# Kernel optimization log

Hardware: AMD Instinct MI355X
Metric: run time of the kernel (lower is better)

Reference implementation:

```python
import jax, jax.numpy as jnp
import numpy as np

N_FILTRATIONS = 24
TEMPERATURE = 0.15
H1_WEIGHT = 0.5
LAMBDA_TOPO = 0.1


def setup_inputs() -> dict:
    key = jax.random.key(0)
    embeddings = jax.random.normal(key, (4096, 512), dtype=jnp.float32)
    return {"embeddings": embeddings, "step": 0}


def _landscape_loss(embeddings):
    N = embeddings.shape[0]
    emb = embeddings.astype(jnp.float32)
    # pairwise euclidean distances (torch.cdist p=2), safe sqrt for grad at 0
    sq = jnp.sum(emb * emb, axis=1)
    d2 = sq[:, None] + sq[None, :] - 2.0 * (emb @ emb.T)
    d2 = jnp.maximum(d2, 0.0)
    pos = d2 > 1e-12
    dist = jnp.where(pos, jnp.sqrt(jnp.where(pos, d2, 1.0)), 0.0)
    eye = jnp.eye(N, dtype=jnp.float32)
    dist = dist + eye * 1e9  # [N, N], diag pushed to 'infinity'
    off = dist < 1e8
    # thresholds come from .item() in torch -> no grad through them
    d_min = jax.lax.stop_gradient(jnp.min(jnp.where(off, dist, jnp.inf)))
    d_max = jax.lax.stop_gradient(
        jnp.maximum(jnp.max(jnp.where(off, dist, -jnp.inf)), d_min + 1e-4))
    thresholds = jnp.linspace(d_min, d_max, N_FILTRATIONS)

    one_minus_eye = 1.0 - eye

    def step_fn(carry, thresh):
        adj = jax.nn.sigmoid((thresh - dist) / TEMPERATURE) * one_minus_eye
        deg = jnp.clip(jnp.sum(adj, axis=-1), 1e-6, None)
        n_isolated = jnp.sum((deg < 0.5).astype(jnp.float32))  # H0 proxy
        n_edges_soft = jnp.sum(adj) / 2.0
        n_excess = jax.nn.relu(n_edges_soft - (N - 1)) / N  # H1 proxy
        return carry, (n_isolated, n_excess)

    _, (h0, h1) = jax.lax.scan(step_fn, None, thresholds)
    h0_loss = jnp.mean(h0[-8:])
    h1_loss = jnp.mean(h1)
    total = h0_loss + H1_WEIGHT * h1_loss
    return total * LAMBDA_TOPO


def reference(embeddings, step) -> jnp.ndarray:
    # warmup_steps = 0, so the warmup skip branch never triggers;
    # N == max_points, so no subsampling.
    return _landscape_loss(embeddings)
```

## Files before the change

kernel.cpp:

```cpp
#include <hip/hip_runtime.h>
#include <stdint.h>

typedef float f32x4 __attribute__((ext_vector_type(4)));
typedef short s16x8 __attribute__((ext_vector_type(8)));
typedef unsigned short us4 __attribute__((ext_vector_type(4)));

#define NPTS 4096
#define DDIM 512
#define NF   24
#define NBLK 32
#define NBD  1024

#define OFF_SQ  4194304
#define OFF_MM  4210688
#define OFF_DEG 4210752
#define OFF_D   4603968
#define OFF_H   38158400ULL
#define WS_A    54935616ULL

typedef __attribute__((address_space(1))) void gvoid;
typedef __attribute__((address_space(3))) void svoid;
#define GLD16(gp, lp) __builtin_amdgcn_global_load_lds((gvoid*)(gp), (svoid*)(lp), 16, 0, 0)

static __device__ __forceinline__ ushort f2h(float x) {
    _Float16 h = (_Float16)x;
    return __builtin_bit_cast(unsigned short, h);
}
static __device__ __forceinline__ float h2f(ushort u) {
    return (float)__builtin_bit_cast(_Float16, u);
}

__global__ __launch_bounds__(256) void k_init(float* __restrict__ deg,
                                              unsigned* __restrict__ mm) {
    int i = blockIdx.x * 256 + threadIdx.x;
    if (i < NPTS * NF) deg[i] = 0.0f;
    if (i == 0) { mm[0] = 0x7F7FFFFFu; mm[1] = 0u; }
}

__global__ __launch_bounds__(256) void k_convert(const float* __restrict__ in,
                                                 ushort* __restrict__ Eb,
                                                 float* __restrict__ sq,
                                                 float* __restrict__ acc32,
                                                 unsigned* __restrict__ mm) {
    if (blockIdx.x == 0) {
        if (threadIdx.x < 32) acc32[threadIdx.x] = 0.0f;
        else if (threadIdx.x == 32) mm[0] = 0x7F7FFFFFu;
        else if (threadIdx.x == 33) mm[1] = 0u;
    }
    const int w = threadIdx.x >> 6, lane = threadIdx.x & 63;
    const int row = blockIdx.x * 4 + w;
    const float* src = in + (size_t)row * DDIM + lane * 8;
    float4 a = ((const float4*)src)[0];
    float4 b = ((const float4*)src)[1];
    float v[8] = {a.x, a.y, a.z, a.w, b.x, b.y, b.z, b.w};
    unsigned u[8];
    float ss = 0.0f;
#pragma unroll
    for (int i = 0; i < 8; ++i) {
        ss += v[i] * v[i];
        unsigned bits = __float_as_uint(v[i]);
        u[i] = (bits + 0x7FFFu + ((bits >> 16) & 1u)) >> 16;
    }
    uint4 pk;
    pk.x = u[0] | (u[1] << 16);
    pk.y = u[2] | (u[3] << 16);
    pk.z = u[4] | (u[5] << 16);
    pk.w = u[6] | (u[7] << 16);
    *(uint4*)(Eb + (size_t)row * DDIM + lane * 8) = pk;
#pragma unroll
    for (int s = 1; s < 64; s <<= 1) ss += __shfl_xor(ss, s);
    if (lane == 0) sq[row] = ss;
}

__global__ __launch_bounds__(256) void k_gram_bk64(const ushort* __restrict__ Eb,
                                                   const float* __restrict__ sq,
                                                   unsigned* __restrict__ mm,
                                                   ushort* __restrict__ D2h) {
    __shared__ __align__(16) ushort SM[32768];
    __shared__ float sqr[128], sqc[128], red[8];
    char* SMb = (char*)SM;
    const int tid = threadIdx.x;
    const int w = tid >> 6, lane = tid & 63, g = lane >> 4, l15 = lane & 15;
    const int wr = w >> 1, wc = w & 1;

    int bid = (blockIdx.x & 7) * 66 + (blockIdx.x >> 3);
    int rb = 0, pre = 0;
    while (pre + (NBLK - rb) <= bid) { pre += NBLK - rb; ++rb; }
    const int cb = rb + (bid - pre);

    if (tid < 128) sqr[tid] = sq[rb * 128 + tid];
    else           sqc[tid - 128] = sq[cb * 128 + (tid - 128)];

    f32x4 acc[4][4];
#pragma unroll
    for (int i = 0; i < 4; ++i)
#pragma unroll
        for (int j = 0; j < 4; ++j) acc[i][j] = (f32x4){0.f, 0.f, 0.f, 0.f};

    const int srow_off = lane >> 3, slch = lane & 7;

#define STAGE64(buf, kk)                                                        \
    {                                                                           \
        const int k0_ = (kk) * 64;                                              \
        _Pragma("unroll")                                                       \
        for (int i_ = 0; i_ < 4; ++i_) {                                        \
            const int r_  = w * 32 + i_ * 8 + srow_off;                         \
            const int ch_ = slch ^ (r_ & 7);                                    \
            GLD16(Eb + (size_t)(rb * 128 + r_) * DDIM + k0_ + ch_ * 8,          \
                  SMb + (buf) * 16384 + (w * 32 + i_ * 8) * 128);               \
            GLD16(Eb + (size_t)(cb * 128 + r_) * DDIM + k0_ + ch_ * 8,          \
                  SMb + 32768 + (buf) * 16384 + (w * 32 + i_ * 8) * 128);       \
        }                                                                       \
    }

    STAGE64(0, 0);
    int cur = 0;
#pragma unroll 1
    for (int kk = 0; kk < 8; ++kk) {
        __syncthreads();
        if (kk < 7) STAGE64(cur ^ 1, kk + 1);
        const char* Ac = SMb + cur * 16384;
        const char* Bc = SMb + 32768 + cur * 16384;
#pragma unroll
        for (int ks = 0; ks < 2; ++ks) {
            s16x8 rf[4], cf[4];
#pragma unroll
            for (int i = 0; i < 4; ++i) {
                const int r = wr * 64 + i * 16 + l15;
                const int slot = (ks * 4 + g) ^ (r & 7);
                rf[i] = *(const s16x8*)(Ac + r * 128 + slot * 16);
            }
#pragma unroll
            for (int j = 0; j < 4; ++j) {
                const int r = wc * 64 + j * 16 + l15;
                const int slot = (ks * 4 + g) ^ (r & 7);
                cf[j] = *(const s16x8*)(Bc + r * 128 + slot * 16);
            }
#pragma unroll
            for (int i = 0; i < 4; ++i)
#pragma unroll
                for (int j = 0; j < 4; ++j)
                    acc[i][j] = __builtin_amdgcn_mfma_f32_16x16x32_bf16(
                        cf[j], rf[i], acc[i][j], 0, 0, 0);
        }
        cur ^= 1;
    }
    __syncthreads();

    ushort* T = SM;
    float mn = 3.4e38f, mx = 0.0f;
#pragma unroll
    for (int i = 0; i < 4; ++i) {
        const int lr = wr * 64 + i * 16 + l15;
        const int trow = rb * 128 + lr;
        const float srv = sqr[lr];
#pragma unroll
        for (int j = 0; j < 4; ++j) {
            const int c0 = wc * 64 + j * 16 + g * 4;
            const int tc0 = cb * 128 + c0;
            ushort h[4];
#pragma unroll
            for (int m = 0; m < 4; ++m) {
                float d2 = srv + sqc[c0 + m] - 2.0f * acc[i][j][m];
                d2 = fmaxf(d2, 0.0f);
                bool diag = (tc0 + m == trow);
                mn = diag ? mn : fminf(mn, d2);
                mx = diag ? mx : fmaxf(mx, d2);
                h[m] = f2h(diag ? 6.0e4f : d2);
            }
            us4 pk4 = {h[0], h[1], h[2], h[3]};
            *(us4*)(T + lr * 136 + c0) = pk4;
        }
    }
#pragma unroll
    for (int s = 1; s < 64; s <<= 1) {
        mn = fminf(mn, __shfl_xor(mn, s));
        mx = fmaxf(mx, __shfl_xor(mx, s));
    }
    if (lane == 0) { red[w] = mn; red[4 + w] = mx; }
    __syncthreads();
    if (tid == 0) {
        mn = fminf(fminf(red[0], red[1]), fminf(red[2], red[3]));
        mx = fmaxf(fmaxf(red[4], red[5]), fmaxf(red[6], red[7]));
        atomicMin(&mm[0], __float_as_uint(mn));
        atomicMax(&mm[1], __float_as_uint(mx));
    }
#pragma unroll
    for (int j = 0; j < 8; ++j) {
        const int c = j * 256 + tid;
        const int row = c >> 4, col8 = (c & 15) * 8;
        uint4 v = *(const uint4*)(T + row * 136 + col8);
        *(uint4*)(D2h + (size_t)(rb * 128 + row) * NPTS + cb * 128 + col8) = v;
    }
    if (rb != cb) {
        __syncthreads();
#pragma unroll
        for (int i = 0; i < 4; ++i) {
            const int lr = wr * 64 + i * 16 + l15;
            const float srv = sqr[lr];
#pragma unroll
            for (int j = 0; j < 4; ++j) {
                const int c0 = wc * 64 + j * 16 + g * 4;
#pragma unroll
                for (int m = 0; m < 4; ++m) {
                    float d2 = srv + sqc[c0 + m] - 2.0f * acc[i][j][m];
                    d2 = fmaxf(d2, 0.0f);
                    T[(c0 + m) * 136 + lr] = f2h(d2);
                }
            }
        }
        __syncthreads();
#pragma unroll
        for (int j2 = 0; j2 < 8; ++j2) {
            const int c = j2 * 256 + tid;
            const int row = c >> 4, col8 = (c & 15) * 8;
            uint4 v = *(const uint4*)(T + row * 136 + col8);
            *(uint4*)(D2h + (size_t)(cb * 128 + row) * NPTS + rb * 128 + col8) = v;
        }
    }
}

__global__ __launch_bounds__(256) void k_hist4(const ushort* __restrict__ D2h,
                                               const unsigned* __restrict__ mm,
                                               ushort* __restrict__ H) {
    __shared__ unsigned Hs[4][NBD + 4];
    const int tid = threadIdx.x, w = tid >> 6, lane = tid & 63;
    const int row0 = blockIdx.x * 4;
    const int row = row0 + w;
    for (int i = tid; i < 4 * (NBD + 4); i += 256) ((unsigned*)Hs)[i] = 0u;
    const float d2min = __uint_as_float(mm[0]);
    const float d2max = __uint_as_float(mm[1]);
    const float sc = (float)NBD / fmaxf(d2max - d2min, 1e-6f);
    __syncthreads();
    const uint4* Dv = (const uint4*)(D2h + (size_t)row * NPTS);
    unsigned* hr = Hs[w];
#pragma unroll
    for (int it = 0; it < 8; ++it) {
        uint4 pk = Dv[it * 64 + lane];
        unsigned pw[4] = {pk.x, pk.y, pk.z, pk.w};
#pragma unroll
        for (int i = 0; i < 4; ++i) {
            float a = h2f((ushort)(pw[i] & 0xFFFFu));
            float b = h2f((ushort)(pw[i] >> 16));
            if (a < 3.0e4f) {
                int ba = (int)fminf(fmaxf((a - d2min) * sc, 0.0f), (float)(NBD - 1));
                atomicAdd(&hr[ba], 1u);
            }
            if (b < 3.0e4f) {
                int bb = (int)fminf(fmaxf((b - d2min) * sc, 0.0f), (float)(NBD - 1));
                atomicAdd(&hr[bb], 1u);
            }
        }
    }
    __syncthreads();
    unsigned* Ho = (unsigned*)(H + (size_t)row0 * NBD);
    for (int i = tid; i < 4 * (NBD / 2); i += 256) {
        const int r = i >> 9, pw_ = i & 511;
        unsigned lo = Hs[r][2 * pw_], hi = Hs[r][2 * pw_ + 1];
        Ho[r * (NBD / 2) + pw_] = (lo & 0xFFFFu) | (hi << 16);
    }
}

__global__ __launch_bounds__(512) void k_dot(const ushort* __restrict__ H,
                                             const unsigned* __restrict__ mm,
                                             float* __restrict__ acc32) {
    __shared__ float Wl[4][NBD];
    __shared__ float degb[8][NF];
    const int tid = threadIdx.x;
    const int wid = tid >> 6, lane = tid & 63;
    const int row = blockIdx.x * 8 + wid;

    const float d2min = __uint_as_float(mm[0]);
    const float d2max = __uint_as_float(mm[1]);
    const float bw    = fmaxf(d2max - d2min, 1e-6f) / (float)NBD;
    const float d_min = d2min > 1e-12f ? sqrtf(d2min) : 0.0f;
    const float d_mx  = d2max > 1e-12f ? sqrtf(d2max) : 0.0f;
    const float d_max = fmaxf(d_mx, d_min + 1e-4f);
    const float stp   = (d_max - d_min) / 23.0f;
    const float S2L   = (1.0f / 0.15f) * 1.44269504f;
    const float Ds2   = stp * S2L;
    const float R     = exp2f(-Ds2);
    const float LIM   = 1073741824.0f;

    float hv[16];
    const ushort* Hr = H + (size_t)row * NBD;
#pragma unroll
    for (int j = 0; j < 4; ++j) {
        uint2 pk = *(const uint2*)(Hr + j * 256 + lane * 4);
        hv[j * 4 + 0] = (float)(pk.x & 0xFFFFu);
        hv[j * 4 + 1] = (float)(pk.x >> 16);
        hv[j * 4 + 2] = (float)(pk.y & 0xFFFFu);
        hv[j * 4 + 3] = (float)(pk.y >> 16);
    }

    float e2[2];
#pragma unroll
    for (int q = 0; q < 2; ++q) {
        const int b = tid * 2 + q;
        const float d2c = d2min + ((float)b + 0.5f) * bw;
        const float db = sqrtf(fmaxf(d2c, 0.0f));
        e2[q] = exp2f(fminf((db - d_min) * S2L, 125.0f));
    }

#pragma unroll 1
    for (int ph = 0; ph < 6; ++ph) {
        __syncthreads();
#pragma unroll
        for (int k = 0; k < 4; ++k) {
            float2 sg;
            sg.x = __builtin_amdgcn_rcpf(1.0f + fminf(e2[0], LIM)); e2[0] *= R;
            sg.y = __builtin_amdgcn_rcpf(1.0f + fminf(e2[1], LIM)); e2[1] *= R;
            *(float2*)(&Wl[k][tid * 2]) = sg;
        }
        __syncthreads();
        float dacc[4];
#pragma unroll
        for (int k = 0; k < 4; ++k) {
            const float* Wr = &Wl[k][0];
            float s = 0.0f;
#pragma unroll
            for (int j = 0; j < 4; ++j) {
                const f32x4 wv = *(const f32x4*)(Wr + j * 256 + lane * 4);
                s += hv[j*4+0]*wv[0] + hv[j*4+1]*wv[1] + hv[j*4+2]*wv[2] + hv[j*4+3]*wv[3];
            }
            dacc[k] = s;
        }
#pragma unroll
        for (int k = 0; k < 4; ++k)
#pragma unroll
            for (int o = 1; o < 64; o <<= 1) dacc[k] += __shfl_xor(dacc[k], o);
        if (lane == 0) {
#pragma unroll
            for (int k = 0; k < 4; ++k) degb[wid][ph * 4 + k] = dacc[k];
        }
    }
    __syncthreads();
    if (tid < NF) {
        float s = 0.0f;
#pragma unroll
        for (int r = 0; r < 8; ++r) s += degb[r][tid];
        atomicAdd(&acc32[tid], s);
    } else if (tid < 32) {
        const int k = 16 + (tid - NF);
        float c = 0.0f;
#pragma unroll
        for (int r = 0; r < 8; ++r) c += (degb[r][k] < 0.5f) ? 1.0f : 0.0f;
        atomicAdd(&acc32[tid], c);
    }
}

__global__ __launch_bounds__(64) void k_final2(const float* __restrict__ acc32,
                                               float* __restrict__ out) {
    if (threadIdx.x == 0) {
        float h1 = 0.0f;
#pragma unroll
        for (int k = 0; k < NF; ++k)
            h1 += fmaxf(acc32[k] * 0.5f - (float)(NPTS - 1), 0.0f) * (1.0f / (float)NPTS);
        float h0 = 0.0f;
#pragma unroll
        for (int k = 0; k < 8; ++k) h0 += acc32[NF + k];
        out[0] = (h0 * 0.125f + 0.5f * (h1 * (1.0f / 24.0f))) * 0.1f;
    }
}

__device__ __forceinline__ void gram_tile(const ushort* __restrict__ Eb, int rb, int cb,
                                          ushort* As, ushort* Bs, f32x4 acc[2][8]) {
    const int tid = threadIdx.x;
    const int w = tid >> 6, lane = tid & 63, g = lane >> 4, l15 = lane & 15;
#pragma unroll 1
    for (int kk = 0; kk < DDIM / 32; ++kk) {
        const int k0 = kk * 32;
        __syncthreads();
#pragma unroll
        for (int it = 0; it < 2; ++it) {
            int li  = it * 256 + tid;
            int row = li >> 2, ch = li & 3;
            uint4 va = *(const uint4*)(Eb + (size_t)(rb * 128 + row) * DDIM + k0 + ch * 8);
            uint4 vb = *(const uint4*)(Eb + (size_t)(cb * 128 + row) * DDIM + k0 + ch * 8);
            *(uint4*)(As + row * 32 + ch * 8) = va;
            *(uint4*)(Bs + row * 32 + ch * 8) = vb;
        }
        __syncthreads();
        s16x8 rf0 = *(const s16x8*)(As + (w * 32 + 0 * 16 + l15) * 32 + g * 8);
        s16x8 rf1 = *(const s16x8*)(As + (w * 32 + 1 * 16 + l15) * 32 + g * 8);
#pragma unroll
        for (int bj = 0; bj < 8; ++bj) {
            s16x8 cf = *(const s16x8*)(Bs + (bj * 16 + l15) * 32 + g * 8);
            acc[0][bj] = __builtin_amdgcn_mfma_f32_16x16x32_bf16(cf, rf0, acc[0][bj], 0, 0, 0);
            acc[1][bj] = __builtin_amdgcn_mfma_f32_16x16x32_bf16(cf, rf1, acc[1][bj], 0, 0, 0);
        }
    }
}

__global__ __launch_bounds__(256) void k_minmax(const ushort* __restrict__ Eb,
                                                const float* __restrict__ sq,
                                                unsigned* __restrict__ mm) {
    const int rb = blockIdx.y, cb = blockIdx.x;
    if (cb < rb) return;
    __shared__ ushort As[128 * 32], Bs[128 * 32];
    __shared__ float sqr[128], sqc[128];
    __shared__ float red[8];
    const int tid = threadIdx.x;
    if (tid < 128) sqr[tid] = sq[rb * 128 + tid];
    else           sqc[tid - 128] = sq[cb * 128 + (tid - 128)];
    f32x4 acc[2][8];
#pragma unroll
    for (int bi = 0; bi < 2; ++bi)
#pragma unroll
        for (int bj = 0; bj < 8; ++bj) acc[bi][bj] = (f32x4){0.f, 0.f, 0.f, 0.f};
    gram_tile(Eb, rb, cb, As, Bs, acc);
    const int w = tid >> 6, lane = tid & 63, g = lane >> 4, l15 = lane & 15;
    const float sr0 = sqr[w * 32 + l15], sr1 = sqr[w * 32 + 16 + l15];
    float mn = 3.4e38f, mx = 0.0f;
#pragma unroll
    for (int bi = 0; bi < 2; ++bi)
#pragma unroll
        for (int bj = 0; bj < 8; ++bj)
#pragma unroll
            for (int m = 0; m < 4; ++m) {
                int tr = w * 32 + bi * 16 + l15;
                int tc = bj * 16 + g * 4 + m;
                float d2 = (bi ? sr1 : sr0) + sqc[tc] - 2.0f * acc[bi][bj][m];
                d2 = fmaxf(d2, 0.0f);
                bool diag = (rb == cb) && (tr == tc);
                mn = diag ? mn : fminf(mn, d2);
                mx = diag ? mx : fmaxf(mx, d2);
            }
#pragma unroll
    for (int s = 1; s < 64; s <<= 1) {
        mn = fminf(mn, __shfl_xor(mn, s));
        mx = fmaxf(mx, __shfl_xor(mx, s));
    }
    if (lane == 0) { red[w] = mn; red[4 + w] = mx; }
    __syncthreads();
    if (tid == 0) {
        mn = fminf(fminf(red[0], red[1]), fminf(red[2], red[3]));
        mx = fmaxf(fmaxf(red[4], red[5]), fmaxf(red[6], red[7]));
        atomicMin(&mm[0], __float_as_uint(mn));
        atomicMax(&mm[1], __float_as_uint(mx));
    }
}

__global__ __launch_bounds__(256) void k_accum2(const ushort* __restrict__ Eb,
                                                const float* __restrict__ sq,
                                                const unsigned* __restrict__ mm,
                                                float* __restrict__ deg) {
    const int rb = blockIdx.y, cb = blockIdx.x;
    __shared__ ushort As[128 * 32], Bs[128 * 32];
    __shared__ float sqr[128], sqc[128];
    __shared__ float degr[128][NF];
    const int tid = threadIdx.x;
    if (tid < 128) sqr[tid] = sq[rb * 128 + tid];
    else           sqc[tid - 128] = sq[cb * 128 + (tid - 128)];
    for (int i = tid; i < 128 * NF; i += 256) ((float*)degr)[i] = 0.0f;
    f32x4 acc[2][8];
#pragma unroll
    for (int bi = 0; bi < 2; ++bi)
#pragma unroll
        for (int bj = 0; bj < 8; ++bj) acc[bi][bj] = (f32x4){0.f, 0.f, 0.f, 0.f};
    gram_tile(Eb, rb, cb, As, Bs, acc);
    const int w = tid >> 6, lane = tid & 63, g = lane >> 4, l15 = lane & 15;

    const float dmin2 = __uint_as_float(mm[0]);
    const float dmax2 = __uint_as_float(mm[1]);
    const float d_min = dmin2 > 1e-12f ? sqrtf(dmin2) : 0.0f;
    const float d_mx  = dmax2 > 1e-12f ? sqrtf(dmax2) : 0.0f;
    const float d_max = fmaxf(d_mx, d_min + 1e-4f);
    const float stp   = (d_max - d_min) / 23.0f;
    const float S2L   = (1.0f / 0.15f) * 1.44269504f;
    const float Ds2   = stp * S2L;
    const float R     = exp2f(-Ds2);
    const float LIM   = 1073741824.0f;
    const float ECAP  = 125.0f;

    const float sr0 = sqr[w * 32 + l15], sr1 = sqr[w * 32 + 16 + l15];
    f32x4 ee[2][8];
#pragma unroll
    for (int bi = 0; bi < 2; ++bi)
#pragma unroll
        for (int bj = 0; bj < 8; ++bj)
#pragma unroll
            for (int m = 0; m < 4; ++m) {
                int tr = w * 32 + bi * 16 + l15;
                int tc = bj * 16 + g * 4 + m;
                float d2 = (bi ? sr1 : sr0) + sqc[tc] - 2.0f * acc[bi][bj][m];
                d2 = fmaxf(d2, 0.0f);
                float d = d2 > 1e-12f ? sqrtf(d2) : 0.0f;
                if (rb == cb && tr == tc) d = 1e9f;
                ee[bi][bj][m] = exp2f(fminf((d - d_min) * S2L, ECAP));
            }

#pragma unroll 1
    for (int t = 0; t < NF; ++t) {
        float rs0 = 0.0f, rs1 = 0.0f;
#pragma unroll
        for (int bj = 0; bj < 8; ++bj) {
            {
                f32x4 q = ee[0][bj];
                float A  = 1.0f + fminf(q.x, LIM), B  = 1.0f + fminf(q.y, LIM);
                float Cq = 1.0f + fminf(q.z, LIM), Dq = 1.0f + fminf(q.w, LIM);
                float sAB = A + B,  sCD = Cq + Dq;
                float pAB = A * B,  pCD = Cq * Dq;
                rs0 += (sAB * pCD + sCD * pAB) * __builtin_amdgcn_rcpf(pAB * pCD);
                ee[0][bj] = q * R;
            }
            {
                f32x4 q = ee[1][bj];
                float A  = 1.0f + fminf(q.x, LIM), B  = 1.0f + fminf(q.y, LIM);
                float Cq = 1.0f + fminf(q.z, LIM), Dq = 1.0f + fminf(q.w, LIM);
                float sAB = A + B,  sCD = Cq + Dq;
                float pAB = A * B,  pCD = Cq * Dq;
                rs1 += (sAB * pCD + sCD * pAB) * __builtin_amdgcn_rcpf(pAB * pCD);
                ee[1][bj] = q * R;
            }
        }
        rs0 += __shfl_xor(rs0, 16); rs0 += __shfl_xor(rs0, 32);
        rs1 += __shfl_xor(rs1, 16); rs1 += __shfl_xor(rs1, 32);
        if (g == 0) {
            degr[w * 32 + l15][t]      += rs0;
            degr[w * 32 + 16 + l15][t] += rs1;
        }
    }
    __syncthreads();
    for (int i = tid; i < 128 * NF; i += 256) {
        int r = i / NF, t = i % NF;
        atomicAdd(&deg[(size_t)(rb * 128 + r) * NF + t], degr[r][t]);
    }
}

__global__ __launch_bounds__(256) void k_final(const float* __restrict__ deg,
                                               float* __restrict__ out) {
    const int tid = threadIdx.x;
    float s[NF], cnt[8];
#pragma unroll
    for (int t = 0; t < NF; ++t) s[t] = 0.0f;
#pragma unroll
    for (int k = 0; k < 8; ++k) cnt[k] = 0.0f;
    for (int i = tid; i < NPTS; i += 256) {
        const float* row = deg + (size_t)i * NF;
#pragma unroll
        for (int t = 0; t < NF; ++t) {
            float v = row[t];
            s[t] += v;
            if (t >= 16) cnt[t - 16] += (v < 0.5f) ? 1.0f : 0.0f;
        }
    }
#pragma unroll
    for (int t = 0; t < NF; ++t)
#pragma unroll
        for (int o = 1; o < 64; o <<= 1) s[t] += __shfl_xor(s[t], o);
#pragma unroll
    for (int k = 0; k < 8; ++k)
#pragma unroll
        for (int o = 1; o < 64; o <<= 1) cnt[k] += __shfl_xor(cnt[k], o);
    __shared__ float red[4][32];
    const int w = tid >> 6, lane = tid & 63;
    if (lane == 0) {
#pragma unroll
        for (int t = 0; t < NF; ++t) red[w][t] = s[t];
#pragma unroll
        for (int k = 0; k < 8; ++k) red[w][NF + k] = cnt[k];
    }
    __syncthreads();
    if (tid == 0) {
        float h0 = 0.0f, h1 = 0.0f;
#pragma unroll
        for (int t = 0; t < NF; ++t) {
            float S = red[0][t] + red[1][t] + red[2][t] + red[3][t];
            float edges = S * 0.5f;
            h1 += fmaxf(edges - (float)(NPTS - 1), 0.0f) / (float)NPTS;
        }
#pragma unroll
        for (int k = 0; k < 8; ++k)
            h0 += red[0][NF + k] + red[1][NF + k] + red[2][NF + k] + red[3][NF + k];
        h0 *= (1.0f / 8.0f);
        h1 *= (1.0f / 24.0f);
        out[0] = (h0 + 0.5f * h1) * 0.1f;
    }
}

extern "C" void kernel_launch(void* const* d_in, const int* in_sizes, int n_in,
                              void* d_out, int out_size, void* d_ws, size_t ws_size,
                              hipStream_t stream) {
    (void)in_sizes; (void)n_in; (void)out_size;
    const float* emb = (const float*)d_in[0];
    uint8_t* ws = (uint8_t*)d_ws;
    ushort*   Eb  = (ushort*)(ws);
    float*    sqv = (float*)(ws + OFF_SQ);
    unsigned* mm  = (unsigned*)(ws + OFF_MM);
    float*    deg = (float*)(ws + OFF_DEG);
    ushort*   D2h = (ushort*)(ws + OFF_D);
    ushort*   H   = (ushort*)(ws + OFF_H);
    float*    out = (float*)d_out;
    const bool bigws = (ws_size >= WS_A);

    if (bigws) {
        k_convert  <<<dim3(NPTS / 4),              dim3(256), 0, stream>>>(emb, Eb, sqv, deg, mm);
        k_gram_bk64<<<dim3(NBLK * (NBLK + 1) / 2), dim3(256), 0, stream>>>(Eb, sqv, mm, D2h);
        k_hist4    <<<dim3(NPTS / 4),              dim3(256), 0, stream>>>(D2h, mm, H);
        k_dot      <<<dim3(NPTS / 8),              dim3(512), 0, stream>>>(H, mm, deg);
        k_final2   <<<dim3(1),                     dim3(64),  0, stream>>>(deg, out);
    } else {
        k_init   <<<dim3(384),      dim3(256), 0, stream>>>(deg, mm);
        k_convert<<<dim3(NPTS / 4), dim3(256), 0, stream>>>(emb, Eb, sqv, deg, mm);
        k_minmax <<<dim3(32, 32),   dim3(256), 0, stream>>>(Eb, sqv, mm);
        k_accum2 <<<dim3(32, 32),   dim3(256), 0, stream>>>(Eb, sqv, mm, deg);
        k_final  <<<dim3(1),        dim3(256), 0, stream>>>(deg, out);
    }
}
```

Before: 74.18 us.

## Fuse histogram, sigmoid dot and final reduction into one kernel

Merges the per-row histogram kernel, the sigmoid-weighted dot kernel and the single-thread final kernel into one 512-thread kernel. Histograms stay in shared memory instead of going through a global 16-bit buffer, and a last-block-done atomic counter (stored in mm[2]) computes the final loss. This removes two launches and a global write/read round trip. In exchange it uses more shared memory per block, which may lower occupancy, and adds a threadfence/counter serialization at the end.

```diff
diff --git a/kernel.cpp b/kernel.cpp
--- a/kernel.cpp
+++ b/kernel.cpp
@@ -15,7 +15,6 @@
 #define OFF_MM  4210688
 #define OFF_DEG 4210752
 #define OFF_D   4603968
-#define OFF_H   38158400ULL
 #define WS_A    54935616ULL
 
 typedef __attribute__((address_space(1))) void gvoid;
@@ -46,6 +45,7 @@
         if (threadIdx.x < 32) acc32[threadIdx.x] = 0.0f;
         else if (threadIdx.x == 32) mm[0] = 0x7F7FFFFFu;
         else if (threadIdx.x == 33) mm[1] = 0u;
+        else if (threadIdx.x == 34) mm[2] = 0u;
     }
     const int w = threadIdx.x >> 6, lane = threadIdx.x & 63;
     const int row = blockIdx.x * 4 + w;
@@ -220,18 +220,23 @@
     }
 }
 
-__global__ __launch_bounds__(256) void k_hist4(const ushort* __restrict__ D2h,
-                                               const unsigned* __restrict__ mm,
-                                               ushort* __restrict__ H) {
-    __shared__ unsigned Hs[4][NBD + 4];
+__global__ __launch_bounds__(512) void k_hd(const ushort* __restrict__ D2h,
+                                            const unsigned* __restrict__ mm_,
+                                            float* __restrict__ acc32,
+                                            float* __restrict__ out) {
+    __shared__ unsigned Hs[8][NBD + 4];
+    __shared__ float Wl[4][NBD];
+    __shared__ float degb[8][NF];
+    unsigned* mm = (unsigned*)mm_;
     const int tid = threadIdx.x, w = tid >> 6, lane = tid & 63;
-    const int row0 = blockIdx.x * 4;
-    const int row = row0 + w;
-    for (int i = tid; i < 4 * (NBD + 4); i += 256) ((unsigned*)Hs)[i] = 0u;
+    const int row = blockIdx.x * 8 + w;
+
+    for (int i = tid; i < 8 * (NBD + 4); i += 512) ((unsigned*)Hs)[i] = 0u;
     const float d2min = __uint_as_float(mm[0]);
     const float d2max = __uint_as_float(mm[1]);
     const float sc = (float)NBD / fmaxf(d2max - d2min, 1e-6f);
     __syncthreads();
+
     const uint4* Dv = (const uint4*)(D2h + (size_t)row * NPTS);
     unsigned* hr = Hs[w];
 #pragma unroll
@@ -253,25 +258,17 @@
         }
     }
     __syncthreads();
-    unsigned* Ho = (unsigned*)(H + (size_t)row0 * NBD);
-    for (int i = tid; i < 4 * (NBD / 2); i += 256) {
-        const int r = i >> 9, pw_ = i & 511;
-        unsigned lo = Hs[r][2 * pw_], hi = Hs[r][2 * pw_ + 1];
-        Ho[r * (NBD / 2) + pw_] = (lo & 0xFFFFu) | (hi << 16);
-    }
-}
-
-__global__ __launch_bounds__(512) void k_dot(const ushort* __restrict__ H,
-                                             const unsigned* __restrict__ mm,
-                                             float* __restrict__ acc32) {
-    __shared__ float Wl[4][NBD];
-    __shared__ float degb[8][NF];
-    const int tid = threadIdx.x;
-    const int wid = tid >> 6, lane = tid & 63;
-    const int row = blockIdx.x * 8 + wid;
-
-    const float d2min = __uint_as_float(mm[0]);
-    const float d2max = __uint_as_float(mm[1]);
+
+    float hv[16];
+#pragma unroll
+    for (int j = 0; j < 4; ++j) {
+        const unsigned* q = &Hs[w][j * 256 + lane * 4];
+        hv[j * 4 + 0] = (float)q[0];
+        hv[j * 4 + 1] = (float)q[1];
+        hv[j * 4 + 2] = (float)q[2];
+        hv[j * 4 + 3] = (float)q[3];
+    }
+
     const float bw    = fmaxf(d2max - d2min, 1e-6f) / (float)NBD;
     const float d_min = d2min > 1e-12f ? sqrtf(d2min) : 0.0f;
     const float d_mx  = d2max > 1e-12f ? sqrtf(d2max) : 0.0f;
@@ -282,17 +279,6 @@
     const float R     = exp2f(-Ds2);
     const float LIM   = 1073741824.0f;
 
-    float hv[16];
-    const ushort* Hr = H + (size_t)row * NBD;
-#pragma unroll
-    for (int j = 0; j < 4; ++j) {
-        uint2 pk = *(const uint2*)(Hr + j * 256 + lane * 4);
-        hv[j * 4 + 0] = (float)(pk.x & 0xFFFFu);
-        hv[j * 4 + 1] = (float)(pk.x >> 16);
-        hv[j * 4 + 2] = (float)(pk.y & 0xFFFFu);
-        hv[j * 4 + 3] = (float)(pk.y >> 16);
-    }
-
     float e2[2];
 #pragma unroll
     for (int q = 0; q < 2; ++q) {
@@ -331,7 +317,7 @@
             for (int o = 1; o < 64; o <<= 1) dacc[k] += __shfl_xor(dacc[k], o);
         if (lane == 0) {
 #pragma unroll
-            for (int k = 0; k < 4; ++k) degb[wid][ph * 4 + k] = dacc[k];
+            for (int k = 0; k < 4; ++k) degb[w][ph * 4 + k] = dacc[k];
         }
     }
     __syncthreads();
@@ -347,19 +333,22 @@
         for (int r = 0; r < 8; ++r) c += (degb[r][k] < 0.5f) ? 1.0f : 0.0f;
         atomicAdd(&acc32[tid], c);
     }
-}
-
-__global__ __launch_bounds__(64) void k_final2(const float* __restrict__ acc32,
-                                               float* __restrict__ out) {
-    if (threadIdx.x == 0) {
-        float h1 = 0.0f;
-#pragma unroll
-        for (int k = 0; k < NF; ++k)
-            h1 += fmaxf(acc32[k] * 0.5f - (float)(NPTS - 1), 0.0f) * (1.0f / (float)NPTS);
-        float h0 = 0.0f;
-#pragma unroll
-        for (int k = 0; k < 8; ++k) h0 += acc32[NF + k];
-        out[0] = (h0 * 0.125f + 0.5f * (h1 * (1.0f / 24.0f))) * 0.1f;
+    __syncthreads();
+    if (tid == 0) {
+        __threadfence();
+        unsigned old = atomicAdd(&mm[2], 1u);
+        if (old == gridDim.x - 1) {
+            __threadfence();
+            volatile float* a = (volatile float*)acc32;
+            float h1 = 0.0f;
+#pragma unroll
+            for (int k = 0; k < NF; ++k)
+                h1 += fmaxf(a[k] * 0.5f - (float)(NPTS - 1), 0.0f) * (1.0f / (float)NPTS);
+            float h0 = 0.0f;
+#pragma unroll
+            for (int k = 0; k < 8; ++k) h0 += a[NF + k];
+            out[0] = (h0 * 0.125f + 0.5f * (h1 * (1.0f / 24.0f))) * 0.1f;
+        }
     }
 }
 
@@ -590,16 +579,13 @@
     unsigned* mm  = (unsigned*)(ws + OFF_MM);
     float*    deg = (float*)(ws + OFF_DEG);
     ushort*   D2h = (ushort*)(ws + OFF_D);
-    ushort*   H   = (ushort*)(ws + OFF_H);
     float*    out = (float*)d_out;
     const bool bigws = (ws_size >= WS_A);
 
     if (bigws) {
         k_convert  <<<dim3(NPTS / 4),              dim3(256), 0, stream>>>(emb, Eb, sqv, deg, mm);
         k_gram_bk64<<<dim3(NBLK * (NBLK + 1) / 2), dim3(256), 0, stream>>>(Eb, sqv, mm, D2h);
-        k_hist4    <<<dim3(NPTS / 4),              dim3(256), 0, stream>>>(D2h, mm, H);
-        k_dot      <<<dim3(NPTS / 8),              dim3(512), 0, stream>>>(H, mm, deg);
-        k_final2   <<<dim3(1),                     dim3(64),  0, stream>>>(deg, out);
+        k_hd       <<<dim3(NPTS / 8),              dim3(512), 0, stream>>>(D2h, mm, deg, out);
     } else {
         k_init   <<<dim3(384),      dim3(256), 0, stream>>>(deg, mm);
         k_convert<<<dim3(NPTS / 4), dim3(256), 0, stream>>>(emb, Eb, sqv, deg, mm);
```

Result: slower. 75.69 us (+2.0%).
